# Kernel optimization log

Measured on AMD Instinct MI355X. Metric: run time of the kernel, lower is better.

Reference implementation:

```python
import jax, jax.numpy as jnp
import numpy as np

EMBED = 256
HEADS = 8
LEVELS = 1
POINTS = 4
NBQ = 2          # num_bev_queue
HBEV = 128
WBEV = 128
BS = 1


def setup_inputs() -> dict:
    key = jax.random.key(0)
    ks = jax.random.split(key, 10)
    Nq = HBEV * WBEV
    E = EMBED
    so_out = NBQ * HEADS * LEVELS * POINTS * 2
    aw_out = NBQ * HEADS * LEVELS * POINTS
    return {
        "query": jax.random.normal(ks[0], (BS, Nq, E), jnp.float32),
        "value": jax.random.normal(ks[1], (BS, NBQ * Nq, E), jnp.float32),
        "reference_points": jax.random.uniform(ks[2], (BS, Nq, LEVELS, 2), jnp.float32),
        # params stored as [in, out]; y = x @ W + b (math-equivalent to torch Linear)
        "W_vproj": jax.random.normal(ks[3], (E, E), jnp.float32) / np.sqrt(E).astype(np.float32),
        "b_vproj": jnp.zeros((E,), jnp.float32),
        "W_so": jax.random.normal(ks[4], (NBQ * E, so_out), jnp.float32) * 0.01,
        "b_so": jax.random.normal(ks[5], (so_out,), jnp.float32) * 0.5,
        "W_aw": jax.random.normal(ks[6], (NBQ * E, aw_out), jnp.float32) * 0.01,
        "b_aw": jnp.zeros((aw_out,), jnp.float32),
        "W_out": jax.random.normal(ks[7], (E, E), jnp.float32) / np.sqrt(E).astype(np.float32),
        "b_out": jnp.zeros((E,), jnp.float32),
        "spatial_shapes": jnp.array([[HBEV, WBEV]], jnp.int32),
        "level_start_index": jnp.array([0], jnp.int32),
    }


def _msda(value, spatial_shapes, sampling_locations, attention_weights):
    """Multi-scale deformable attention (grid_sample semantics: bilinear,
    zero padding, align_corners=False).
    value: [B, sum(H*W), Hh, d]; sampling_locations: [B, Nq, Hh, L, P, 2] in [0,1];
    attention_weights: [B, Nq, Hh, L, P]. Returns [B, Nq, Hh*d]."""
    B, _, Hh, d = value.shape
    _, Nq, _, L, P, _ = sampling_locations.shape
    ss = np.asarray(spatial_shapes)
    out = jnp.zeros((B, Nq, Hh, d), value.dtype)
    start = 0
    for l in range(L):
        H_, W_ = int(ss[l, 0]), int(ss[l, 1])
        v = value[:, start:start + H_ * W_]          # [B, H*W, Hh, d]
        start += H_ * W_
        loc = sampling_locations[:, :, :, l]          # [B, Nq, Hh, P, 2]
        # align_corners=False: pixel = loc*size - 0.5
        px = loc[..., 0] * W_ - 0.5
        py = loc[..., 1] * H_ - 0.5
        x0f = jnp.floor(px)
        y0f = jnp.floor(py)
        lx = px - x0f
        ly = py - y0f
        x0 = x0f.astype(jnp.int32)
        y0 = y0f.astype(jnp.int32)

        def gather(ix, iy):
            valid = ((ix >= 0) & (ix < W_) & (iy >= 0) & (iy < H_))
            idx = jnp.clip(iy, 0, H_ - 1) * W_ + jnp.clip(ix, 0, W_ - 1)   # [B,Nq,Hh,P]
            idx = jnp.transpose(idx, (0, 1, 3, 2)).reshape(B, Nq * P, Hh, 1)
            g = jnp.take_along_axis(v, idx, axis=1).reshape(B, Nq, P, Hh, d)
            m = jnp.transpose(valid, (0, 1, 3, 2))[..., None].astype(value.dtype)
            return g * m

        def wmul(w):  # [B,Nq,Hh,P] -> [B,Nq,P,Hh,1]
            return jnp.transpose(w, (0, 1, 3, 2))[..., None]

        sampled = (wmul((1 - lx) * (1 - ly)) * gather(x0, y0)
                   + wmul(lx * (1 - ly)) * gather(x0 + 1, y0)
                   + wmul((1 - lx) * ly) * gather(x0, y0 + 1)
                   + wmul(lx * ly) * gather(x0 + 1, y0 + 1))   # [B,Nq,P,Hh,d]
        out = out + jnp.einsum('bqphd,bqhp->bqhd', sampled, attention_weights[:, :, :, l])
    return out.reshape(B, Nq, Hh * d)


def reference(query, value, reference_points, W_vproj, b_vproj, W_so, b_so,
              W_aw, b_aw, W_out, b_out, spatial_shapes, level_start_index):
    bs, Nq, E = query.shape
    Hh, L, P, nbq = HEADS, LEVELS, POINTS, NBQ
    identity = query
    # query enhanced with the previous-BEV slice of value
    qe = jnp.concatenate([value[:, :Nq], query], axis=-1)        # [bs, Nq, 2E]
    v = (value @ W_vproj + b_vproj).reshape(bs * nbq, Nq, Hh, E // Hh)
    so = (qe @ W_so + b_so).reshape(bs, Nq, Hh, nbq, L, P, 2)
    aw = jax.nn.softmax((qe @ W_aw + b_aw).reshape(bs, Nq, Hh, nbq, L * P), axis=-1)
    aw = aw.reshape(bs, Nq, Hh, nbq, L, P)
    aw = jnp.transpose(aw, (0, 3, 1, 2, 4, 5)).reshape(bs * nbq, Nq, Hh, L, P)
    so = jnp.transpose(so, (0, 3, 1, 2, 4, 5, 6)).reshape(bs * nbq, Nq, Hh, L, P, 2)
    rp = jnp.tile(reference_points, (nbq, 1, 1, 1))              # [bs*nbq, Nq, L, 2]
    ssf = spatial_shapes.astype(so.dtype)
    offset_normalizer = jnp.stack([ssf[:, 1], ssf[:, 0]], -1)    # [L, 2] = (W, H)
    loc = rp[:, :, None, :, None, :] + so / offset_normalizer[None, None, None, :, None, :]
    out = _msda(v, spatial_shapes, loc, aw).reshape(bs, nbq, Nq, E).mean(axis=1)
    out = out @ W_out + b_out
    return out + identity  # dropout is identity in eval mode
```

## Files before the change

### kernel.cpp

```cpp
#include <hip/hip_runtime.h>
#include <math.h>

#define NQ     16384
#define NHEAD  8
#define GW     128
#define GH     128

typedef __attribute__((ext_vector_type(8))) short short8;
typedef __attribute__((ext_vector_type(4))) float f32x4;

static __device__ __forceinline__ unsigned short f2bf(float f) {
    unsigned u = __builtin_bit_cast(unsigned, f);
    u += 0x7FFFu + ((u >> 16) & 1u);
    return (unsigned short)(u >> 16);
}
static __device__ __forceinline__ unsigned pk2(float lo, float hi) {
    return (unsigned)f2bf(lo) | ((unsigned)f2bf(hi) << 16);
}

__global__ void prep(const float* __restrict__ Wv, const float* __restrict__ Wso,
                     const float* __restrict__ Waw, const float* __restrict__ bso,
                     const float* __restrict__ baw, const float* __restrict__ Wo,
                     unsigned short* __restrict__ WTv, unsigned short* __restrict__ WTso,
                     unsigned short* __restrict__ WTo, float* __restrict__ bias2)
{
    const int n = blockIdx.x;
    const int k = threadIdx.x;
    WTv[n * 256 + k] = f2bf(Wv[(size_t)k * 256 + n]);
    WTo[n * 256 + k] = f2bf(Wo[(size_t)k * 256 + n]);
    float s0, s1;
    if (n < 128)      { s0 = Wso[(size_t)k * 128 + n];       s1 = Wso[(size_t)(k + 256) * 128 + n]; }
    else if (n < 192) { s0 = Waw[(size_t)k * 64 + n - 128];  s1 = Waw[(size_t)(k + 256) * 64 + n - 128]; }
    else              { s0 = 0.f; s1 = 0.f; }
    WTso[(size_t)n * 512 + k]       = f2bf(s0);
    WTso[(size_t)n * 512 + k + 256] = f2bf(s1);
    if (k == 0) bias2[n] = (n < 128) ? bso[n] : ((n < 192) ? baw[n - 128] : 0.f);
}

template<int KTOT, int MODE>
__global__ __launch_bounds__(256, 2)
void gemm_mfma(const float* __restrict__ A1, const float* __restrict__ A2,
               const unsigned short* __restrict__ Abf,
               const unsigned short* __restrict__ WT,
               const float* __restrict__ bias, const float* __restrict__ resid,
               void* __restrict__ Cout)
{
    __shared__ __align__(16) unsigned short As[8 * 128 * 8];
    __shared__ __align__(16) unsigned short Bs[8 * 128 * 8];

    const int tid = threadIdx.x;
    const int m0 = blockIdx.x * 128;
    const int n0 = blockIdx.y * 128;
    const int w = tid >> 6, lane = tid & 63;
    const int wr = w >> 1, wc = w & 1;
    const int g = lane >> 4, r16 = lane & 15;

    f32x4 acc[4][4] = {};

    for (int k0 = 0; k0 < KTOT; k0 += 64) {
        if (MODE == 2) {
            #pragma unroll
            for (int c = 0; c < 4; ++c) {
                int idx = tid + c * 256;
                int row = idx >> 3, oct = idx & 7;
                uint4 wv = *reinterpret_cast<const uint4*>(
                    &Abf[(size_t)(m0 + row) * 256 + k0 + oct * 8]);
                *reinterpret_cast<uint4*>(&As[(oct * 128 + row) * 8]) = wv;
            }
        } else {
            const float* Asrc = (KTOT == 512 && k0 >= 256) ? (A2 + (k0 - 256)) : (A1 + k0);
            #pragma unroll
            for (int c = 0; c < 4; ++c) {
                int idx = tid + c * 256;
                int row = idx >> 3, oct = idx & 7;
                const float* p = Asrc + (size_t)(m0 + row) * 256 + oct * 8;
                float4 f0 = *reinterpret_cast<const float4*>(p);
                float4 f1 = *reinterpret_cast<const float4*>(p + 4);
                uint4 wv;
                wv.x = pk2(f0.x, f0.y); wv.y = pk2(f0.z, f0.w);
                wv.z = pk2(f1.x, f1.y); wv.w = pk2(f1.z, f1.w);
                *reinterpret_cast<uint4*>(&As[(oct * 128 + row) * 8]) = wv;
            }
        }
        #pragma unroll
        for (int c = 0; c < 4; ++c) {
            int idx = tid + c * 256;
            int n = idx >> 3, oct = idx & 7;
            uint4 wv = *reinterpret_cast<const uint4*>(
                &WT[(size_t)(n0 + n) * KTOT + k0 + oct * 8]);
            *reinterpret_cast<uint4*>(&Bs[(oct * 128 + n) * 8]) = wv;
        }
        __syncthreads();

        #pragma unroll
        for (int kh = 0; kh < 2; ++kh) {
            short8 af[4], bfr[4];
            #pragma unroll
            for (int m = 0; m < 4; ++m)
                af[m] = *reinterpret_cast<const short8*>(
                    &As[(((kh * 4 + g) * 128) + wr * 64 + m * 16 + r16) * 8]);
            #pragma unroll
            for (int n = 0; n < 4; ++n)
                bfr[n] = *reinterpret_cast<const short8*>(
                    &Bs[(((kh * 4 + g) * 128) + wc * 64 + n * 16 + r16) * 8]);
            #pragma unroll
            for (int m = 0; m < 4; ++m)
                #pragma unroll
                for (int n = 0; n < 4; ++n)
                    acc[m][n] = __builtin_amdgcn_mfma_f32_16x16x32_bf16(
                        af[m], bfr[n], acc[m][n], 0, 0, 0);
        }
        __syncthreads();
    }

    #pragma unroll
    for (int m = 0; m < 4; ++m) {
        int row = m0 + wr * 64 + m * 16 + g * 4;
        #pragma unroll
        for (int n = 0; n < 4; ++n) {
            int col = n0 + wc * 64 + n * 16 + r16;
            if (MODE == 1 && col >= 192) continue;
            float bia = bias[col];
            #pragma unroll
            for (int j = 0; j < 4; ++j) {
                float vo = acc[m][n][j] + bia;
                if (MODE == 0) {
                    ((unsigned short*)Cout)[(size_t)(row + j) * 256 + col] = f2bf(vo);
                } else if (MODE == 1) {
                    ((float*)Cout)[(size_t)(row + j) * 192 + col] = vo;
                } else {
                    ((float*)Cout)[(size_t)(row + j) * 256 + col] =
                        vo + resid[(size_t)(row + j) * 256 + col];
                }
            }
        }
    }
}

static __device__ __forceinline__ void acc4(f32x4& acc, float w, uint2 r) {
    acc[0] = fmaf(w, __builtin_bit_cast(float, r.x << 16), acc[0]);
    acc[1] = fmaf(w, __builtin_bit_cast(float, r.x & 0xffff0000u), acc[1]);
    acc[2] = fmaf(w, __builtin_bit_cast(float, r.y << 16), acc[2]);
    acc[3] = fmaf(w, __builtin_bit_cast(float, r.y & 0xffff0000u), acc[3]);
}

__global__ __launch_bounds__(256)
void sampler(const unsigned short* __restrict__ v, const float* __restrict__ soaw,
             const float* __restrict__ rp, unsigned short* __restrict__ outm)
{
    __shared__ float so_s[4][128];
    __shared__ float w_s[4][64];

    const int t = threadIdx.x;
    const int wv = t >> 6, ln = t & 63;
    const int q = blockIdx.x * 4 + wv;
    const float* row = soaw + (size_t)q * 192;

    so_s[wv][ln]      = row[ln];
    so_s[wv][64 + ln] = row[64 + ln];
    float a = row[128 + ln];
    float m = fmaxf(a, __shfl_xor(a, 1, 4));
    m = fmaxf(m, __shfl_xor(m, 2, 4));
    float e = __expf(a - m);
    float s = e + __shfl_xor(e, 1, 4);
    s += __shfl_xor(s, 2, 4);
    w_s[wv][ln] = e / s;
    __syncthreads();

    const float rpx = rp[q * 2 + 0], rpy = rp[q * 2 + 1];
    const int h = ln >> 3, c = ln & 7;
    const int sub = h * 64 + c * 8;
    f32x4 acc = {0.f, 0.f, 0.f, 0.f};

    #pragma unroll
    for (int b = 0; b < 2; ++b) {
        const char* vb = (const char*)v + (size_t)b * NQ * 512;
        #pragma unroll
        for (int p = 0; p < 4; ++p) {
            float sox = so_s[wv][h * 16 + b * 8 + p * 2 + 0];
            float soy = so_s[wv][h * 16 + b * 8 + p * 2 + 1];
            float wbp = w_s[wv][h * 8 + b * 4 + p];
            float px = (rpx + sox * (1.0f / 128.0f)) * 128.0f - 0.5f;
            float py = (rpy + soy * (1.0f / 128.0f)) * 128.0f - 0.5f;
            float x0f = floorf(px), y0f = floorf(py);
            float lx = px - x0f, ly = py - y0f;
            int x0 = (int)x0f, y0 = (int)y0f;
            int x1 = x0 + 1, y1 = y0 + 1;
            float wx0 = (1.f - lx) * ((x0 >= 0 && x0 < GW) ? 1.f : 0.f);
            float wx1 = lx         * ((x1 >= 0 && x1 < GW) ? 1.f : 0.f);
            float wy0 = (1.f - ly) * ((y0 >= 0 && y0 < GH) ? 1.f : 0.f);
            float wy1 = ly         * ((y1 >= 0 && y1 < GH) ? 1.f : 0.f);
            int x0c = min(max(x0, 0), GW - 1), x1c = min(max(x1, 0), GW - 1);
            int y0c = min(max(y0, 0), GH - 1), y1c = min(max(y1, 0), GH - 1);
            uint2 r00 = *(const uint2*)(vb + ((y0c * GW + x0c) * 512 + sub));
            uint2 r10 = *(const uint2*)(vb + ((y0c * GW + x1c) * 512 + sub));
            uint2 r01 = *(const uint2*)(vb + ((y1c * GW + x0c) * 512 + sub));
            uint2 r11 = *(const uint2*)(vb + ((y1c * GW + x1c) * 512 + sub));
            acc4(acc, wbp * wx0 * wy0, r00);
            acc4(acc, wbp * wx1 * wy0, r10);
            acc4(acc, wbp * wx0 * wy1, r01);
            acc4(acc, wbp * wx1 * wy1, r11);
        }
    }

    uint2 o;
    o.x = pk2(0.5f * acc[0], 0.5f * acc[1]);
    o.y = pk2(0.5f * acc[2], 0.5f * acc[3]);
    *reinterpret_cast<uint2*>(&outm[(size_t)q * 256 + h * 32 + c * 4]) = o;
}

extern "C" void kernel_launch(void* const* d_in, const int* in_sizes, int n_in,
                              void* d_out, int out_size, void* d_ws, size_t ws_size,
                              hipStream_t stream)
{
    const float* query   = (const float*)d_in[0];
    const float* value   = (const float*)d_in[1];
    const float* rp      = (const float*)d_in[2];
    const float* W_vproj = (const float*)d_in[3];
    const float* b_vproj = (const float*)d_in[4];
    const float* W_so    = (const float*)d_in[5];
    const float* b_so    = (const float*)d_in[6];
    const float* W_aw    = (const float*)d_in[7];
    const float* b_aw    = (const float*)d_in[8];
    const float* W_out   = (const float*)d_in[9];
    const float* b_out   = (const float*)d_in[10];
    float* out = (float*)d_out;

    char* wp = (char*)d_ws;
    unsigned short* ws_v    = (unsigned short*)wp; wp += (size_t)2 * NQ * 256 * 2;
    float*          ws_soaw = (float*)wp;          wp += (size_t)NQ * 192 * 4;
    unsigned short* ws_mean = (unsigned short*)wp; wp += (size_t)NQ * 256 * 2;
    unsigned short* WTv     = (unsigned short*)wp; wp += 256 * 256 * 2;
    unsigned short* WTso    = (unsigned short*)wp; wp += 256 * 512 * 2;
    unsigned short* WTo     = (unsigned short*)wp; wp += 256 * 256 * 2;
    float*          bias2   = (float*)wp;          wp += 256 * 4;

    prep<<<dim3(256), dim3(256), 0, stream>>>(W_vproj, W_so, W_aw, b_so, b_aw, W_out,
                                              WTv, WTso, WTo, bias2);
    gemm_mfma<256, 0><<<dim3(256, 2), dim3(256), 0, stream>>>(
        value, nullptr, nullptr, WTv, b_vproj, nullptr, ws_v);
    gemm_mfma<512, 1><<<dim3(128, 2), dim3(256), 0, stream>>>(
        value, query, nullptr, WTso, bias2, nullptr, ws_soaw);
    sampler<<<dim3(NQ / 4), dim3(256), 0, stream>>>(ws_v, ws_soaw, rp, ws_mean);
    gemm_mfma<256, 2><<<dim3(128, 2), dim3(256), 0, stream>>>(
        nullptr, nullptr, ws_mean, WTo, b_out, query, out);
}
```

Baseline: 84.44 us.

## Merge value and offset GEMMs into one launch; widen sampler loads

Combines the value-projection GEMM and the offset/attention-weight GEMM into a single grid of 768 blocks. This removes a launch and lets the two independent GEMMs run concurrently and fill the GPU. The sampler now handles 8 queries per block with 32 lanes per query, and each lane gathers 16 bytes (8 channels) per corner instead of 8 bytes. Softmax is computed per thread over 4 contiguous logits, and blocks are remapped with a swizzled query order, presumably to improve cache locality. The cost is more registers per sampler thread and a different grid mapping.

```diff
diff --git a/kernel.cpp b/kernel.cpp
--- a/kernel.cpp
+++ b/kernel.cpp
@@ -16,6 +16,12 @@
 }
 static __device__ __forceinline__ unsigned pk2(float lo, float hi) {
     return (unsigned)f2bf(lo) | ((unsigned)f2bf(hi) << 16);
+}
+static __device__ __forceinline__ float bflo(unsigned u) {
+    return __builtin_bit_cast(float, u << 16);
+}
+static __device__ __forceinline__ float bfhi(unsigned u) {
+    return __builtin_bit_cast(float, u & 0xffff0000u);
 }
 
 __global__ void prep(const float* __restrict__ Wv, const float* __restrict__ Wso,
@@ -38,19 +44,16 @@
 }
 
 template<int KTOT, int MODE>
-__global__ __launch_bounds__(256, 2)
-void gemm_mfma(const float* __restrict__ A1, const float* __restrict__ A2,
-               const unsigned short* __restrict__ Abf,
-               const unsigned short* __restrict__ WT,
-               const float* __restrict__ bias, const float* __restrict__ resid,
-               void* __restrict__ Cout)
-{
-    __shared__ __align__(16) unsigned short As[8 * 128 * 8];
-    __shared__ __align__(16) unsigned short Bs[8 * 128 * 8];
-
+static __device__ __forceinline__ void gemm_body(
+    int m0, int n0,
+    const float* __restrict__ A1, const float* __restrict__ A2,
+    const unsigned short* __restrict__ Abf,
+    const unsigned short* __restrict__ WT,
+    const float* __restrict__ bias, const float* __restrict__ resid,
+    void* __restrict__ Cout,
+    unsigned short* As, unsigned short* Bs)
+{
     const int tid = threadIdx.x;
-    const int m0 = blockIdx.x * 128;
-    const int n0 = blockIdx.y * 128;
     const int w = tid >> 6, lane = tid & 63;
     const int wr = w >> 1, wc = w & 1;
     const int g = lane >> 4, r16 = lane & 15;
@@ -137,49 +140,98 @@
     }
 }
 
-static __device__ __forceinline__ void acc4(f32x4& acc, float w, uint2 r) {
-    acc[0] = fmaf(w, __builtin_bit_cast(float, r.x << 16), acc[0]);
-    acc[1] = fmaf(w, __builtin_bit_cast(float, r.x & 0xffff0000u), acc[1]);
-    acc[2] = fmaf(w, __builtin_bit_cast(float, r.y << 16), acc[2]);
-    acc[3] = fmaf(w, __builtin_bit_cast(float, r.y & 0xffff0000u), acc[3]);
+__global__ __launch_bounds__(256, 2)
+void gemm_vs(const float* __restrict__ value, const float* __restrict__ query,
+             const unsigned short* __restrict__ WTv, const unsigned short* __restrict__ WTso,
+             const float* __restrict__ bv, const float* __restrict__ bias2,
+             unsigned short* __restrict__ v_out, float* __restrict__ soaw_out)
+{
+    __shared__ __align__(16) unsigned short As[8 * 128 * 8];
+    __shared__ __align__(16) unsigned short Bs[8 * 128 * 8];
+    const int bid = blockIdx.x;
+    if (bid < 512) {
+        gemm_body<256, 0>((bid >> 1) * 128, (bid & 1) * 128,
+                          value, nullptr, nullptr, WTv, bv, nullptr, v_out, As, Bs);
+    } else {
+        const int b2 = bid - 512;
+        gemm_body<512, 1>((b2 >> 1) * 128, (b2 & 1) * 128,
+                          value, query, nullptr, WTso, bias2, nullptr, soaw_out, As, Bs);
+    }
+}
+
+__global__ __launch_bounds__(256, 2)
+void gemm_out(const unsigned short* __restrict__ Abf, const unsigned short* __restrict__ WTo,
+              const float* __restrict__ bo, const float* __restrict__ resid,
+              float* __restrict__ out)
+{
+    __shared__ __align__(16) unsigned short As[8 * 128 * 8];
+    __shared__ __align__(16) unsigned short Bs[8 * 128 * 8];
+    const int bid = blockIdx.x;
+    gemm_body<256, 2>((bid >> 1) * 128, (bid & 1) * 128,
+                      nullptr, nullptr, Abf, WTo, bo, resid, out, As, Bs);
+}
+
+static __device__ __forceinline__ void acc8(float* acc, float w, uint4 r) {
+    acc[0] = fmaf(w, bflo(r.x), acc[0]);
+    acc[1] = fmaf(w, bfhi(r.x), acc[1]);
+    acc[2] = fmaf(w, bflo(r.y), acc[2]);
+    acc[3] = fmaf(w, bfhi(r.y), acc[3]);
+    acc[4] = fmaf(w, bflo(r.z), acc[4]);
+    acc[5] = fmaf(w, bfhi(r.z), acc[5]);
+    acc[6] = fmaf(w, bflo(r.w), acc[6]);
+    acc[7] = fmaf(w, bfhi(r.w), acc[7]);
 }
 
 __global__ __launch_bounds__(256)
 void sampler(const unsigned short* __restrict__ v, const float* __restrict__ soaw,
              const float* __restrict__ rp, unsigned short* __restrict__ outm)
 {
-    __shared__ float so_s[4][128];
-    __shared__ float w_s[4][64];
+    __shared__ float so_s[8][128];
+    __shared__ float w_s[8][64];
+    __shared__ float rp_s[8][2];
 
     const int t = threadIdx.x;
-    const int wv = t >> 6, ln = t & 63;
-    const int q = blockIdx.x * 4 + wv;
-    const float* row = soaw + (size_t)q * 192;
-
-    so_s[wv][ln]      = row[ln];
-    so_s[wv][64 + ln] = row[64 + ln];
-    float a = row[128 + ln];
-    float m = fmaxf(a, __shfl_xor(a, 1, 4));
-    m = fmaxf(m, __shfl_xor(m, 2, 4));
-    float e = __expf(a - m);
-    float s = e + __shfl_xor(e, 1, 4);
-    s += __shfl_xor(s, 2, 4);
-    w_s[wv][ln] = e / s;
+    const int bid = blockIdx.x;
+    const int q0 = ((bid & 7) * 256 + (bid >> 3)) * 8;
+
+    #pragma unroll
+    for (int i = 0; i < 4; ++i) {
+        int idx = t + i * 256;
+        int qq = idx >> 7, off = idx & 127;
+        so_s[qq][off] = soaw[(size_t)(q0 + qq) * 192 + off];
+    }
+    if (t < 128) {
+        int qq = t >> 4, grp = t & 15;
+        float4 a4 = *reinterpret_cast<const float4*>(
+            &soaw[(size_t)(q0 + qq) * 192 + 128 + grp * 4]);
+        float m = fmaxf(fmaxf(a4.x, a4.y), fmaxf(a4.z, a4.w));
+        float e0 = __expf(a4.x - m), e1 = __expf(a4.y - m);
+        float e2 = __expf(a4.z - m), e3 = __expf(a4.w - m);
+        float inv = 1.f / (e0 + e1 + e2 + e3);
+        w_s[qq][grp * 4 + 0] = e0 * inv;
+        w_s[qq][grp * 4 + 1] = e1 * inv;
+        w_s[qq][grp * 4 + 2] = e2 * inv;
+        w_s[qq][grp * 4 + 3] = e3 * inv;
+    }
+    if (t < 16) rp_s[t >> 1][t & 1] = rp[(size_t)(q0 + (t >> 1)) * 2 + (t & 1)];
     __syncthreads();
 
-    const float rpx = rp[q * 2 + 0], rpy = rp[q * 2 + 1];
-    const int h = ln >> 3, c = ln & 7;
-    const int sub = h * 64 + c * 8;
-    f32x4 acc = {0.f, 0.f, 0.f, 0.f};
+    const int wq = t >> 5;
+    const int q = q0 + wq;
+    const int s = t & 31;
+    const int h = s >> 2, c = s & 3;
+    const int sub = h * 64 + c * 16;
+    const float rpx = rp_s[wq][0], rpy = rp_s[wq][1];
+    float acc[8] = {};
 
     #pragma unroll
     for (int b = 0; b < 2; ++b) {
         const char* vb = (const char*)v + (size_t)b * NQ * 512;
         #pragma unroll
         for (int p = 0; p < 4; ++p) {
-            float sox = so_s[wv][h * 16 + b * 8 + p * 2 + 0];
-            float soy = so_s[wv][h * 16 + b * 8 + p * 2 + 1];
-            float wbp = w_s[wv][h * 8 + b * 4 + p];
+            float sox = so_s[wq][h * 16 + b * 8 + p * 2 + 0];
+            float soy = so_s[wq][h * 16 + b * 8 + p * 2 + 1];
+            float wbp = w_s[wq][h * 8 + b * 4 + p];
             float px = (rpx + sox * (1.0f / 128.0f)) * 128.0f - 0.5f;
             float py = (rpy + soy * (1.0f / 128.0f)) * 128.0f - 0.5f;
             float x0f = floorf(px), y0f = floorf(py);
@@ -192,21 +244,23 @@
             float wy1 = ly         * ((y1 >= 0 && y1 < GH) ? 1.f : 0.f);
             int x0c = min(max(x0, 0), GW - 1), x1c = min(max(x1, 0), GW - 1);
             int y0c = min(max(y0, 0), GH - 1), y1c = min(max(y1, 0), GH - 1);
-            uint2 r00 = *(const uint2*)(vb + ((y0c * GW + x0c) * 512 + sub));
-            uint2 r10 = *(const uint2*)(vb + ((y0c * GW + x1c) * 512 + sub));
-            uint2 r01 = *(const uint2*)(vb + ((y1c * GW + x0c) * 512 + sub));
-            uint2 r11 = *(const uint2*)(vb + ((y1c * GW + x1c) * 512 + sub));
-            acc4(acc, wbp * wx0 * wy0, r00);
-            acc4(acc, wbp * wx1 * wy0, r10);
-            acc4(acc, wbp * wx0 * wy1, r01);
-            acc4(acc, wbp * wx1 * wy1, r11);
-        }
-    }
-
-    uint2 o;
+            uint4 r00 = *(const uint4*)(vb + ((size_t)(y0c * GW + x0c) * 512 + sub));
+            uint4 r10 = *(const uint4*)(vb + ((size_t)(y0c * GW + x1c) * 512 + sub));
+            uint4 r01 = *(const uint4*)(vb + ((size_t)(y1c * GW + x0c) * 512 + sub));
+            uint4 r11 = *(const uint4*)(vb + ((size_t)(y1c * GW + x1c) * 512 + sub));
+            acc8(acc, wbp * wx0 * wy0, r00);
+            acc8(acc, wbp * wx1 * wy0, r10);
+            acc8(acc, wbp * wx0 * wy1, r01);
+            acc8(acc, wbp * wx1 * wy1, r11);
+        }
+    }
+
+    uint4 o;
     o.x = pk2(0.5f * acc[0], 0.5f * acc[1]);
     o.y = pk2(0.5f * acc[2], 0.5f * acc[3]);
-    *reinterpret_cast<uint2*>(&outm[(size_t)q * 256 + h * 32 + c * 4]) = o;
+    o.z = pk2(0.5f * acc[4], 0.5f * acc[5]);
+    o.w = pk2(0.5f * acc[6], 0.5f * acc[7]);
+    *reinterpret_cast<uint4*>((char*)outm + (size_t)q * 512 + sub) = o;
 }
 
 extern "C" void kernel_launch(void* const* d_in, const int* in_sizes, int n_in,
@@ -237,11 +291,8 @@
 
     prep<<<dim3(256), dim3(256), 0, stream>>>(W_vproj, W_so, W_aw, b_so, b_aw, W_out,
                                               WTv, WTso, WTo, bias2);
-    gemm_mfma<256, 0><<<dim3(256, 2), dim3(256), 0, stream>>>(
-        value, nullptr, nullptr, WTv, b_vproj, nullptr, ws_v);
-    gemm_mfma<512, 1><<<dim3(128, 2), dim3(256), 0, stream>>>(
-        value, query, nullptr, WTso, bias2, nullptr, ws_soaw);
-    sampler<<<dim3(NQ / 4), dim3(256), 0, stream>>>(ws_v, ws_soaw, rp, ws_mean);
-    gemm_mfma<256, 2><<<dim3(128, 2), dim3(256), 0, stream>>>(
-        nullptr, nullptr, ws_mean, WTo, b_out, query, out);
-}
+    gemm_vs<<<dim3(768), dim3(256), 0, stream>>>(value, query, WTv, WTso,
+                                                 b_vproj, bias2, ws_v, ws_soaw);
+    sampler<<<dim3(NQ / 8), dim3(256), 0, stream>>>(ws_v, ws_soaw, rp, ws_mean);
+    gemm_out<<<dim3(256), dim3(256), 0, stream>>>(ws_mean, WTo, b_out, query, out);
+}
```

Measured after the change: 95.53 us. +13.1%, slower.
